# Kernel tuning notes

Hardware: AMD Instinct MI355X
Metric: run time of the kernel (lower is better)

Reference implementation:

```python
import jax, jax.numpy as jnp
import numpy as np

B, D_IN = 16384, 1024
N_DOM, EMB = 4, 16
H1, H2, H3 = 512, 256, 128
FH = 64
EPS = 1e-5


def setup_inputs() -> dict:
    key = jax.random.key(0)
    ks = jax.random.split(key, 32)
    s = 0.02
    def rn(k, shape):
        return jax.random.normal(k, shape, dtype=jnp.float32) * s
    inp = {
        "x": jax.random.normal(ks[0], (B, D_IN), dtype=jnp.float32),
        "domain_ids": jax.random.randint(ks[1], (B,), 0, N_DOM),
        # PartitionedNormalization params
        "pn_w": jnp.ones((N_DOM, D_IN), jnp.float32),
        "pn_b": jnp.zeros((N_DOM, D_IN), jnp.float32),
        # center net: D_IN->512->256->128
        "cW1": rn(ks[2], (D_IN, H1)), "cb1": jnp.zeros((H1,), jnp.float32),
        "cW2": rn(ks[3], (H1, H2)),  "cb2": jnp.zeros((H2,), jnp.float32),
        "cW3": rn(ks[4], (H2, H3)),  "cb3": jnp.zeros((H3,), jnp.float32),
        # domain-specific nets, stacked over domains
        "dW1": rn(ks[5], (N_DOM, D_IN, H1)), "db1": jnp.zeros((N_DOM, H1), jnp.float32),
        "dW2": rn(ks[6], (N_DOM, H1, H2)),  "db2": jnp.zeros((N_DOM, H2), jnp.float32),
        "dW3": rn(ks[7], (N_DOM, H2, H3)),  "db3": jnp.full((N_DOM, H3), 1.0, jnp.float32),  # domain_net_init_bias=1.0
        # final mlp: 128->64->1
        "fW1": rn(ks[8], (H3, FH)), "fb1": jnp.zeros((FH,), jnp.float32),
        "fW2": rn(ks[9], (FH, 1)),  "fb2": jnp.zeros((1,), jnp.float32),
        # domain embedding + auxiliary net: 16->32->1
        "dom_emb": rn(ks[10], (N_DOM, EMB)),
        "aW1": rn(ks[11], (EMB, 32)), "ab1": jnp.zeros((32,), jnp.float32),
        "aW2": rn(ks[12], (32, 1)),   "ab2": jnp.zeros((1,), jnp.float32),
    }
    return inp


def _forward(x, domain_ids, pn_w, pn_b,
             cW1, cb1, cW2, cb2, cW3, cb3,
             dW1, db1, dW2, db2, dW3, db3,
             fW1, fb1, fW2, fb2,
             dom_emb, aW1, ab1, aW2, ab2):
    # Partitioned normalization: per-sample layernorm over features,
    # domain-conditional affine (vectorized gather instead of python loop)
    mean = jnp.mean(x, axis=1, keepdims=True)
    var = jnp.mean(jnp.square(x - mean), axis=1, keepdims=True)  # unbiased=False
    norm = (x - mean) / jnp.sqrt(var + EPS)
    norm = norm * pn_w[domain_ids] + pn_b[domain_ids]  # (B, D_IN)

    # center net
    h = jax.nn.relu(norm @ cW1 + cb1)
    h = jax.nn.relu(h @ cW2 + cb2)
    h_center = h @ cW3 + cb3  # (B, H3)

    # domain-specific nets: compute all domains, then gather per-sample
    hd = jax.nn.relu(jnp.einsum('bi,dio->bdo', norm, dW1) + db1[None])   # (B,D,H1)
    hd = jax.nn.relu(jnp.einsum('bdi,dio->bdo', hd, dW2) + db2[None])    # (B,D,H2)
    hd = jnp.einsum('bdi,dio->bdo', hd, dW3) + db3[None]                 # (B,D,H3)
    h_domain = jnp.take_along_axis(hd, domain_ids[:, None, None], axis=1)[:, 0]  # (B,H3)

    h_fused = h_center * jnp.tanh(h_domain)

    main = jax.nn.relu(h_fused @ fW1 + fb1) @ fW2 + fb2  # (B,1)

    de = dom_emb[domain_ids]                              # (B,EMB)
    aux = jax.nn.relu(de @ aW1 + ab1) @ aW2 + ab2         # (B,1)

    return jax.nn.sigmoid(main + aux)


def reference(x, domain_ids, pn_w, pn_b,
              cW1, cb1, cW2, cb2, cW3, cb3,
              dW1, db1, dW2, db2, dW3, db3,
              fW1, fb1, fW2, fb2,
              dom_emb, aW1, ab1, aW2, ab2):
    return _forward(x, domain_ids, pn_w, pn_b,
                    cW1, cb1, cW2, cb2, cW3, cb3,
                    dW1, db1, dW2, db2, dW3, db3,
                    fW1, fb1, fW2, fb2,
                    dom_emb, aW1, ab1, aW2, ab2)
```

## Files before the change

kernel.cpp:

```cpp
#include <hip/hip_runtime.h>
#include <hip/hip_bf16.h>
#include <stdint.h>

#define NB   16384
#define DIN  1024
#define MPAD 16896

typedef __bf16 bf16;
typedef __bf16 v8bf __attribute__((ext_vector_type(8)));
typedef float  v4f  __attribute__((ext_vector_type(4)));
typedef long   v2l  __attribute__((ext_vector_type(2)));
typedef unsigned char u8;

typedef __attribute__((address_space(1))) void* as1_ptr;
typedef __attribute__((address_space(3))) void* as3_ptr;

__device__ __forceinline__ void gl_lds16(const void* g, void* l) {
  __builtin_amdgcn_global_load_lds((as1_ptr)(g), (as3_ptr)(l), 16, 0, 0);
}

__device__ __forceinline__ unsigned short bfbits(float f) {
  bf16 h = (bf16)f;
  return __builtin_bit_cast(unsigned short, h);
}

__device__ __forceinline__ unsigned short pk8(float a, float b) {
  int u = __builtin_amdgcn_cvt_pk_fp8_f32(a, b, 0, false);
  return (unsigned short)(u & 0xffff);
}

__global__ __launch_bounds__(1024) void k_histscan_aux(
    const int* __restrict__ dom, int* __restrict__ pstart, int* __restrict__ cnt2,
    int* __restrict__ perm, float* __restrict__ aux,
    const float* __restrict__ dom_emb, const float* __restrict__ aW1,
    const float* __restrict__ ab1, const float* __restrict__ aW2,
    const float* __restrict__ ab2) {
  __shared__ int hist[4];
  int tid = threadIdx.x, lane = tid & 63;
  if (tid < 4) hist[tid] = 0;
  if (tid >= 8 && tid < 12) cnt2[tid - 8] = 0;
  for (int j = tid; j < MPAD; j += 1024) perm[j] = -1;
  __syncthreads();
  int c0 = 0, c1 = 0, c2 = 0, c3 = 0;
#pragma unroll
  for (int it = 0; it < 16; it++) {
    int d = dom[it * 1024 + tid];
    c0 += (d == 0); c1 += (d == 1); c2 += (d == 2); c3 += (d == 3);
  }
#pragma unroll
  for (int o = 32; o; o >>= 1) {
    c0 += __shfl_xor(c0, o, 64); c1 += __shfl_xor(c1, o, 64);
    c2 += __shfl_xor(c2, o, 64); c3 += __shfl_xor(c3, o, 64);
  }
  if (lane == 0) {
    atomicAdd(&hist[0], c0); atomicAdd(&hist[1], c1);
    atomicAdd(&hist[2], c2); atomicAdd(&hist[3], c3);
  }
  __syncthreads();
  if (tid == 0) {
    int p = 0;
    for (int d = 0; d < 4; d++) { pstart[d] = p; p += (hist[d] + 127) & ~127; }
    pstart[4] = p;
  }
  if (tid < 4) {
    float a = ab2[0];
    for (int j = 0; j < 32; j++) {
      float s = ab1[j];
      for (int i = 0; i < 16; i++) s += dom_emb[tid * 16 + i] * aW1[i * 32 + j];
      a += fmaxf(s, 0.f) * aW2[j];
    }
    aux[tid] = a;
  }
}

__global__ void k_assign(const int* __restrict__ dom, const int* __restrict__ pstart,
                         int* __restrict__ cnt2, int* __restrict__ perm,
                         int* __restrict__ rowpos) {
  int i = blockIdx.x * 256 + threadIdx.x;
  int lane = threadIdx.x & 63;
  int d = dom[i];
  unsigned long long ltmask = (1ull << lane) - 1ull;
#pragma unroll
  for (int dd = 0; dd < 4; dd++) {
    unsigned long long m = __ballot(d == dd);
    int c = __popcll(m);
    int base = 0;
    if (lane == 0 && c) base = atomicAdd(&cnt2[dd], c);
    base = __shfl(base, 0, 64);
    if (d == dd) {
      int pos = pstart[dd] + base + __popcll(m & ltmask);
      perm[pos] = i;
      rowpos[i] = pos;
    }
  }
}

__global__ __launch_bounds__(256) void k_ln(const float* __restrict__ x,
                                            const int* __restrict__ dom,
                                            const int* __restrict__ rowpos,
                                            const float* __restrict__ pn_w,
                                            const float* __restrict__ pn_b,
                                            u8* __restrict__ norm) {
  int wv = threadIdx.x >> 6, lane = threadIdx.x & 63;
  int r = blockIdx.x * 4 + wv;
  const float* xr = x + (size_t)r * DIN;
  float4 v[4];
#pragma unroll
  for (int g = 0; g < 4; g++) v[g] = *(const float4*)(xr + g * 256 + lane * 4);
  float s = 0.f;
#pragma unroll
  for (int g = 0; g < 4; g++) s += v[g].x + v[g].y + v[g].z + v[g].w;
#pragma unroll
  for (int o = 32; o; o >>= 1) s += __shfl_xor(s, o, 64);
  float mean = s * (1.f / 1024.f);
  float q = 0.f;
#pragma unroll
  for (int g = 0; g < 4; g++) {
    float a = v[g].x - mean, b = v[g].y - mean, c = v[g].z - mean, e = v[g].w - mean;
    q += a * a + b * b + c * c + e * e;
  }
#pragma unroll
  for (int o = 32; o; o >>= 1) q += __shfl_xor(q, o, 64);
  float rstd = rsqrtf(q * (1.f / 1024.f) + 1e-5f);
  int d = dom[r];
  int pos = rowpos[r];
  const float* pw = pn_w + (size_t)d * DIN;
  const float* pb = pn_b + (size_t)d * DIN;
  u8* orow = norm + (size_t)pos * DIN;
#pragma unroll
  for (int g = 0; g < 4; g++) {
    float4 w4 = *(const float4*)(pw + g * 256 + lane * 4);
    float4 b4 = *(const float4*)(pb + g * 256 + lane * 4);
    float f0 = (v[g].x - mean) * rstd * w4.x + b4.x;
    float f1 = (v[g].y - mean) * rstd * w4.y + b4.y;
    float f2 = (v[g].z - mean) * rstd * w4.z + b4.z;
    float f3 = (v[g].w - mean) * rstd * w4.w + b4.w;
    int u = __builtin_amdgcn_cvt_pk_fp8_f32(f0, f1, 0, false);
    u = __builtin_amdgcn_cvt_pk_fp8_f32(f2, f3, u, true);
    *(unsigned int*)(orow + g * 256 + lane * 4) = (unsigned int)u;
  }
}

__global__ __launch_bounds__(256) void k_wt_all(
    const float* __restrict__ cW1, const float* __restrict__ cW2,
    const float* __restrict__ cW3, const float* __restrict__ dW1,
    const float* __restrict__ dW2, const float* __restrict__ dW3,
    const float* __restrict__ fW1,
    u8* __restrict__ cW1t, u8* __restrict__ cW2t, u8* __restrict__ cW3t,
    u8* __restrict__ dW1t, u8* __restrict__ dW2t, u8* __restrict__ dW3t,
    bf16* __restrict__ fW1t) {
  __shared__ float t[64 * 65];
  int bid = blockIdx.x;
  const float* src; u8* dst; int K, N, tile; bool isf = false;
  if (bid < 640) {
    K = 1024; N = 512; int m = bid >> 7; tile = bid & 127;
    src = m == 0 ? cW1 : dW1 + (size_t)(m - 1) * 524288;
    dst = m == 0 ? cW1t : dW1t + (size_t)(m - 1) * 524288;
  } else if (bid < 800) {
    K = 512; N = 256; int m = (bid - 640) >> 5; tile = (bid - 640) & 31;
    src = m == 0 ? cW2 : dW2 + (size_t)(m - 1) * 131072;
    dst = m == 0 ? cW2t : dW2t + (size_t)(m - 1) * 131072;
  } else if (bid < 840) {
    K = 256; N = 128; int m = (bid - 800) >> 3; tile = (bid - 800) & 7;
    src = m == 0 ? cW3 : dW3 + (size_t)(m - 1) * 32768;
    dst = m == 0 ? cW3t : dW3t + (size_t)(m - 1) * 32768;
  } else {
    K = 128; N = 64; tile = bid - 840; src = fW1; dst = nullptr; isf = true;
  }
  int ntn = N >> 6;
  int k0 = (tile / ntn) << 6, n0 = (tile % ntn) << 6;
  int tid = threadIdx.x;
  int r = tid >> 2, c4 = (tid & 3) << 4;
#pragma unroll
  for (int j4 = 0; j4 < 4; j4++) {
    float4 v = *(const float4*)(src + (size_t)(k0 + r) * N + n0 + c4 + j4 * 4);
    t[r * 65 + c4 + j4 * 4 + 0] = v.x;
    t[r * 65 + c4 + j4 * 4 + 1] = v.y;
    t[r * 65 + c4 + j4 * 4 + 2] = v.z;
    t[r * 65 + c4 + j4 * 4 + 3] = v.w;
  }
  __syncthreads();
  int n = tid >> 2, kc = (tid & 3) << 4;
  if (!isf) {
#pragma unroll
    for (int j4 = 0; j4 < 4; j4++) {
      float v0 = t[(kc + j4 * 4 + 0) * 65 + n] * 16.f;
      float v1 = t[(kc + j4 * 4 + 1) * 65 + n] * 16.f;
      float v2 = t[(kc + j4 * 4 + 2) * 65 + n] * 16.f;
      float v3 = t[(kc + j4 * 4 + 3) * 65 + n] * 16.f;
      int u = __builtin_amdgcn_cvt_pk_fp8_f32(v0, v1, 0, false);
      u = __builtin_amdgcn_cvt_pk_fp8_f32(v2, v3, u, true);
      *(unsigned int*)(dst + (size_t)(n0 + n) * K + k0 + kc + j4 * 4) = (unsigned int)u;
    }
  } else {
#pragma unroll
    for (int j4 = 0; j4 < 4; j4++) {
      ushort4 o;
      o.x = bfbits(t[(kc + j4 * 4 + 0) * 65 + n]);
      o.y = bfbits(t[(kc + j4 * 4 + 1) * 65 + n]);
      o.z = bfbits(t[(kc + j4 * 4 + 2) * 65 + n]);
      o.w = bfbits(t[(kc + j4 * 4 + 3) * 65 + n]);
      *(ushort4*)(fW1t + (size_t)(n0 + n) * K + k0 + kc + j4 * 4) = o;
    }
  }
}

__global__ __launch_bounds__(256) void k_gemm(const u8* __restrict__ A, int lda,
                                              int aoffc, int aoffd,
                                              const u8* __restrict__ cWt,
                                              const u8* __restrict__ dWt,
                                              const float* __restrict__ cb,
                                              const float* __restrict__ db,
                                              u8* __restrict__ C, int Nh, int Kd,
                                              int relu, const int* __restrict__ pstart,
                                              int lognct) {
  __shared__ __align__(16) u8 Al[64 * 128];
  __shared__ __align__(16) u8 Bl[128 * 128];
  const int tid = threadIdx.x;
  const int wv = tid >> 6, lane = tid & 63;
  const int nct = 1 << lognct;
  int l = blockIdx.x;
  int t = l >> 3;
  int ct = t & (nct - 1);
  int rt = ((t >> lognct) << 3) | (l & 7);
  const int row0 = rt * 64;
  const int d = (row0 >= pstart[1]) + (row0 >= pstart[2]) + (row0 >= pstart[3]);
  const int n0 = ct * 128;
  const bool isd = (n0 >= Nh);
  const u8* Wt = isd ? dWt + ((size_t)d * Nh + (n0 - Nh)) * Kd : cWt + (size_t)n0 * Kd;
  const float* bias = isd ? db + d * Nh + (n0 - Nh) : cb + n0;
  const int aoff = isd ? aoffd : aoffc;
  const u8* Ab = A + (size_t)row0 * lda + aoff;

  v4f acc[2][4];
#pragma unroll
  for (int i = 0; i < 2; i++)
#pragma unroll
    for (int j = 0; j < 4; j++) acc[i][j] = v4f{0.f, 0.f, 0.f, 0.f};

  const int wm = (wv >> 1) * 32, wn = (wv & 1) * 64;
  const int mrow = lane & 15, quad = lane >> 4;
  const int lrow = lane >> 3;
  const int lchk = lane & 7;
  const int ldc = 2 * Nh;

  for (int kt = 0; kt < Kd; kt += 128) {
#pragma unroll
    for (int p = 0; p < 2; p++) {
      int rbase = wv * 16 + p * 8;
      int r = rbase + lrow;
      int jg = lchk ^ (r & 7);
      gl_lds16(Ab + (size_t)r * lda + kt + jg * 16, &Al[rbase * 128]);
    }
#pragma unroll
    for (int p = 0; p < 4; p++) {
      int rbase = wv * 32 + p * 8;
      int r = rbase + lrow;
      int jg = lchk ^ (r & 7);
      gl_lds16(Wt + (size_t)r * Kd + kt + jg * 16, &Bl[rbase * 128]);
    }
    __syncthreads();
#pragma unroll
    for (int sp = 0; sp < 2; sp++) {
      v2l af[2], bfr[4];
#pragma unroll
      for (int mi = 0; mi < 2; mi++) {
        int m = wm + mi * 16 + mrow;
        int c = (sp * 4 + quad) ^ (m & 7);
        af[mi] = *(const v2l*)&Al[m * 128 + c * 16];
      }
#pragma unroll
      for (int ni = 0; ni < 4; ni++) {
        int n = wn + ni * 16 + mrow;
        int c = (sp * 4 + quad) ^ (n & 7);
        bfr[ni] = *(const v2l*)&Bl[n * 128 + c * 16];
      }
#pragma unroll
      for (int mi = 0; mi < 2; mi++)
#pragma unroll
        for (int ni = 0; ni < 4; ni++)
          acc[mi][ni] =
              __builtin_amdgcn_mfma_f32_16x16x32_fp8_fp8(af[mi].x, bfr[ni].x, acc[mi][ni], 0, 0, 0);
#pragma unroll
      for (int mi = 0; mi < 2; mi++)
#pragma unroll
        for (int ni = 0; ni < 4; ni++)
          acc[mi][ni] =
              __builtin_amdgcn_mfma_f32_16x16x32_fp8_fp8(af[mi].y, bfr[ni].y, acc[mi][ni], 0, 0, 0);
    }
    __syncthreads();
  }

  float bv[4];
#pragma unroll
  for (int ni = 0; ni < 4; ni++) bv[ni] = bias[wn + ni * 16 + mrow];
#pragma unroll
  for (int mi = 0; mi < 2; mi++) {
    int growb = row0 + wm + mi * 16 + quad * 4;
#pragma unroll
    for (int ni = 0; ni < 4; ni++) {
      int gcol = n0 + wn + ni * 16 + mrow;
#pragma unroll
      for (int r2 = 0; r2 < 4; r2++) {
        float v = acc[mi][ni][r2] * 0.0625f + bv[ni];
        if (relu) v = fmaxf(v, 0.f);
        float g = __shfl_xor(v, 1, 64);
        if (!(mrow & 1))
          *(unsigned short*)(C + (size_t)(growb + r2) * ldc + gcol) = pk8(v, g);
      }
    }
  }
}

__global__ __launch_bounds__(256) void k_gemm3(const u8* __restrict__ A,
                                               const u8* __restrict__ cW3t,
                                               const u8* __restrict__ dW3t,
                                               const float* __restrict__ cb3,
                                               const float* __restrict__ db3,
                                               const bf16* __restrict__ fW1t,
                                               const float* __restrict__ fb1,
                                               const float* __restrict__ fW2,
                                               const float* __restrict__ fb2,
                                               const int* __restrict__ perm,
                                               const int* __restrict__ pstart,
                                               const float* __restrict__ aux,
                                               float* __restrict__ out) {
  __shared__ __align__(16) u8 Al[64 * 128];
  __shared__ __align__(16) u8 Bl[128 * 128];
  __shared__ __align__(16) bf16 fusedL[64 * 128];
  __shared__ __align__(16) bf16 fwB[64 * 128];
  const int tid = threadIdx.x, wv = tid >> 6, lane = tid & 63;
  const int row0 = blockIdx.x * 64;
  const int d = (row0 >= pstart[1]) + (row0 >= pstart[2]) + (row0 >= pstart[3]);
  const u8* Ab = A + (size_t)row0 * 512;
  const int mrow = lane & 15, quad = lane >> 4;
  const int lrow = lane >> 3, lchk = lane & 7;
  const int wm = (wv >> 1) * 32, wn = (wv & 1) * 64;

  {
    int c = lane & 15, rsub = lane >> 4;
#pragma unroll
    for (int p = 0; p < 4; p++) {
      int rbase = wv * 16 + p * 4;
      int row = rbase + rsub;
      int g = (c & 8) | ((c ^ row) & 7);
      gl_lds16(fW1t + row * 128 + g * 8, &fwB[rbase * 128]);
    }
  }

  v4f accC[2][4], accD[2][4];
#pragma unroll
  for (int i = 0; i < 2; i++)
#pragma unroll
    for (int j = 0; j < 4; j++) { accC[i][j] = v4f{0.f,0.f,0.f,0.f}; accD[i][j] = v4f{0.f,0.f,0.f,0.f}; }

#pragma unroll
  for (int ph = 0; ph < 2; ph++) {
    const u8* Wt = ph ? dW3t + (size_t)d * 32768 : cW3t;
    const int aoff = ph * 256;
    for (int kt = 0; kt < 256; kt += 128) {
#pragma unroll
      for (int p = 0; p < 2; p++) {
        int rbase = wv * 16 + p * 8;
        int r = rbase + lrow;
        int jg = lchk ^ (r & 7);
        gl_lds16(Ab + (size_t)r * 512 + aoff + kt + jg * 16, &Al[rbase * 128]);
      }
#pragma unroll
      for (int p = 0; p < 4; p++) {
        int rbase = wv * 32 + p * 8;
        int r = rbase + lrow;
        int jg = lchk ^ (r & 7);
        gl_lds16(Wt + (size_t)r * 256 + kt + jg * 16, &Bl[rbase * 128]);
      }
      __syncthreads();
#pragma unroll
      for (int sp = 0; sp < 2; sp++) {
        v2l af[2], bfr[4];
#pragma unroll
        for (int mi = 0; mi < 2; mi++) {
          int m = wm + mi * 16 + mrow;
          int c = (sp * 4 + quad) ^ (m & 7);
          af[mi] = *(const v2l*)&Al[m * 128 + c * 16];
        }
#pragma unroll
        for (int ni = 0; ni < 4; ni++) {
          int n = wn + ni * 16 + mrow;
          int c = (sp * 4 + quad) ^ (n & 7);
          bfr[ni] = *(const v2l*)&Bl[n * 128 + c * 16];
        }
        if (ph == 0) {
#pragma unroll
          for (int mi = 0; mi < 2; mi++)
#pragma unroll
            for (int ni = 0; ni < 4; ni++) {
              accC[mi][ni] = __builtin_amdgcn_mfma_f32_16x16x32_fp8_fp8(af[mi].x, bfr[ni].x, accC[mi][ni], 0, 0, 0);
              accC[mi][ni] = __builtin_amdgcn_mfma_f32_16x16x32_fp8_fp8(af[mi].y, bfr[ni].y, accC[mi][ni], 0, 0, 0);
            }
        } else {
#pragma unroll
          for (int mi = 0; mi < 2; mi++)
#pragma unroll
            for (int ni = 0; ni < 4; ni++) {
              accD[mi][ni] = __builtin_amdgcn_mfma_f32_16x16x32_fp8_fp8(af[mi].x, bfr[ni].x, accD[mi][ni], 0, 0, 0);
              accD[mi][ni] = __builtin_amdgcn_mfma_f32_16x16x32_fp8_fp8(af[mi].y, bfr[ni].y, accD[mi][ni], 0, 0, 0);
            }
        }
      }
      __syncthreads();
    }
  }

#pragma unroll
  for (int mi = 0; mi < 2; mi++) {
    int rowb = wm + mi * 16 + quad * 4;
#pragma unroll
    for (int ni = 0; ni < 4; ni++) {
      int col = wn + ni * 16 + mrow;
      float cbv = cb3[col];
      float dbv = db3[d * 128 + col];
      int jc = col >> 3, coff = col & 7;
#pragma unroll
      for (int r2 = 0; r2 < 4; r2++) {
        int rr = rowb + r2;
        float f = (accC[mi][ni][r2] * 0.0625f + cbv) * tanhf(accD[mi][ni][r2] * 0.0625f + dbv);
        int cs = (jc & 8) | ((jc ^ rr) & 7);
        fusedL[rr * 128 + cs * 8 + coff] = (bf16)f;
      }
    }
  }
  __syncthreads();

  float fb1v[4], fW2v[4];
#pragma unroll
  for (int nt = 0; nt < 4; nt++) {
    int col = nt * 16 + mrow;
    fb1v[nt] = fb1[col];
    fW2v[nt] = fW2[col];
  }
  v4f hacc[4];
#pragma unroll
  for (int nt = 0; nt < 4; nt++) hacc[nt] = v4f{0.f, 0.f, 0.f, 0.f};
  const int m = wv * 16 + mrow;
#pragma unroll
  for (int s = 0; s < 4; s++) {
    int j = s * 4 + quad;
    int ca = (j & 8) | ((j ^ m) & 7);
    v8bf af = *(const v8bf*)&fusedL[m * 128 + ca * 8];
#pragma unroll
    for (int nt = 0; nt < 4; nt++) {
      int n = nt * 16 + mrow;
      int cbk = (j & 8) | ((j ^ n) & 7);
      v8bf bfr = *(const v8bf*)&fwB[n * 128 + cbk * 8];
      hacc[nt] = __builtin_amdgcn_mfma_f32_16x16x32_bf16(af, bfr, hacc[nt], 0, 0, 0);
    }
  }
  float ys[4];
#pragma unroll
  for (int r2 = 0; r2 < 4; r2++) {
    float s = 0.f;
#pragma unroll
    for (int nt = 0; nt < 4; nt++) s += fmaxf(hacc[nt][r2] + fb1v[nt], 0.f) * fW2v[nt];
    ys[r2] = s;
  }
#pragma unroll
  for (int o = 1; o < 16; o <<= 1)
#pragma unroll
    for (int r2 = 0; r2 < 4; r2++) ys[r2] += __shfl_xor(ys[r2], o, 64);
  if (mrow == 0) {
    const float addc = fb2[0] + aux[d];
#pragma unroll
    for (int r2 = 0; r2 < 4; r2++) {
      int prow = row0 + wv * 16 + quad * 4 + r2;
      int orig = perm[prow];
      if (orig >= 0) out[orig] = 1.f / (1.f + expf(-(ys[r2] + addc)));
    }
  }
}

extern "C" void kernel_launch(void* const* d_in, const int* in_sizes, int n_in,
                              void* d_out, int out_size, void* d_ws, size_t ws_size,
                              hipStream_t stream) {
  (void)in_sizes; (void)n_in; (void)out_size; (void)ws_size;
  const float* x      = (const float*)d_in[0];
  const int*   dom    = (const int*)d_in[1];
  const float* pn_w   = (const float*)d_in[2];
  const float* pn_b   = (const float*)d_in[3];
  const float* cW1    = (const float*)d_in[4];
  const float* cb1    = (const float*)d_in[5];
  const float* cW2    = (const float*)d_in[6];
  const float* cb2    = (const float*)d_in[7];
  const float* cW3    = (const float*)d_in[8];
  const float* cb3    = (const float*)d_in[9];
  const float* dW1    = (const float*)d_in[10];
  const float* db1    = (const float*)d_in[11];
  const float* dW2    = (const float*)d_in[12];
  const float* db2    = (const float*)d_in[13];
  const float* dW3    = (const float*)d_in[14];
  const float* db3    = (const float*)d_in[15];
  const float* fW1    = (const float*)d_in[16];
  const float* fb1    = (const float*)d_in[17];
  const float* fW2    = (const float*)d_in[18];
  const float* fb2    = (const float*)d_in[19];
  const float* demb   = (const float*)d_in[20];
  const float* aW1    = (const float*)d_in[21];
  const float* ab1    = (const float*)d_in[22];
  const float* aW2    = (const float*)d_in[23];
  const float* ab2    = (const float*)d_in[24];
  float* out = (float*)d_out;

  char* w = (char*)d_ws;
  int*   cnt2   = (int*)(w + 0);
  int*   pstart = (int*)(w + 32);
  float* aux    = (float*)(w + 64);
  int*   perm   = (int*)(w + 256);
  int*   rowpos = (int*)(w + 67840);
  u8*    bufA   = (u8*)(w + 133376);
  u8*    bufB   = (u8*)(w + 17434880);
  u8*    cW1t   = (u8*)(w + 34736384);
  u8*    cW2t   = (u8*)(w + 35260672);
  u8*    cW3t   = (u8*)(w + 35391744);
  u8*    dW1t   = (u8*)(w + 35424512);
  u8*    dW2t   = (u8*)(w + 37521664);
  u8*    dW3t   = (u8*)(w + 38045952);
  bf16*  fW1t   = (bf16*)(w + 38177024);

  k_histscan_aux<<<1, 1024, 0, stream>>>(dom, pstart, cnt2, perm, aux,
                                         demb, aW1, ab1, aW2, ab2);
  k_assign<<<64, 256, 0, stream>>>(dom, pstart, cnt2, perm, rowpos);
  k_ln<<<4096, 256, 0, stream>>>(x, dom, rowpos, pn_w, pn_b, bufA);
  k_wt_all<<<842, 256, 0, stream>>>(cW1, cW2, cW3, dW1, dW2, dW3, fW1,
                                    cW1t, cW2t, cW3t, dW1t, dW2t, dW3t, fW1t);

  k_gemm<<<2112, 256, 0, stream>>>(bufA, 1024, 0, 0, cW1t, dW1t, cb1, db1,
                                   bufB, 512, 1024, 1, pstart, 3);
  k_gemm<<<1056, 256, 0, stream>>>(bufB, 1024, 0, 512, cW2t, dW2t, cb2, db2,
                                   bufA, 256, 512, 1, pstart, 2);
  k_gemm3<<<264, 256, 0, stream>>>(bufA, cW3t, dW3t, cb3, db3, fW1t,
                                   fb1, fW2, fb2, perm, pstart, aux, out);
}
```

Measured before the change: 235.1 us.

## Use K=128 scaled FP8 MFMA and parallelize histogram prologue

The GEMM inner loops switch from pairs of 16x16x32 FP8 MFMAs to a single 16x16x128 scaled FP8 MFMA (f8f6f4 with unit scales) per tile, loading 32 contiguous bytes per lane from the swizzled LDS. This cuts MFMA issue count and LDS-read instruction count per K-tile. The single-block histogram/scan/aux kernel is split into a 64-block ballot histogram plus a tiny scan kernel. Counter zeroing and the aux MLP move into a spare block of the weight-transpose kernel, which now runs first. The new path relies on the operand layout of the larger MFMA matching the per-lane chunk selection, and it adds one extra kernel launch.

```diff
diff --git a/kernel.cpp b/kernel.cpp
--- a/kernel.cpp
+++ b/kernel.cpp
@@ -9,7 +9,8 @@
 typedef __bf16 bf16;
 typedef __bf16 v8bf __attribute__((ext_vector_type(8)));
 typedef float  v4f  __attribute__((ext_vector_type(4)));
-typedef long   v2l  __attribute__((ext_vector_type(2)));
+typedef int    v4i  __attribute__((ext_vector_type(4)));
+typedef int    v8i  __attribute__((ext_vector_type(8)));
 typedef unsigned char u8;
 
 typedef __attribute__((address_space(1))) void* as1_ptr;
@@ -29,47 +30,31 @@
   return (unsigned short)(u & 0xffff);
 }
 
-__global__ __launch_bounds__(1024) void k_histscan_aux(
-    const int* __restrict__ dom, int* __restrict__ pstart, int* __restrict__ cnt2,
-    int* __restrict__ perm, float* __restrict__ aux,
-    const float* __restrict__ dom_emb, const float* __restrict__ aW1,
-    const float* __restrict__ ab1, const float* __restrict__ aW2,
-    const float* __restrict__ ab2) {
-  __shared__ int hist[4];
-  int tid = threadIdx.x, lane = tid & 63;
-  if (tid < 4) hist[tid] = 0;
-  if (tid >= 8 && tid < 12) cnt2[tid - 8] = 0;
-  for (int j = tid; j < MPAD; j += 1024) perm[j] = -1;
-  __syncthreads();
-  int c0 = 0, c1 = 0, c2 = 0, c3 = 0;
-#pragma unroll
-  for (int it = 0; it < 16; it++) {
-    int d = dom[it * 1024 + tid];
-    c0 += (d == 0); c1 += (d == 1); c2 += (d == 2); c3 += (d == 3);
-  }
-#pragma unroll
-  for (int o = 32; o; o >>= 1) {
-    c0 += __shfl_xor(c0, o, 64); c1 += __shfl_xor(c1, o, 64);
-    c2 += __shfl_xor(c2, o, 64); c3 += __shfl_xor(c3, o, 64);
-  }
-  if (lane == 0) {
-    atomicAdd(&hist[0], c0); atomicAdd(&hist[1], c1);
-    atomicAdd(&hist[2], c2); atomicAdd(&hist[3], c3);
-  }
-  __syncthreads();
-  if (tid == 0) {
+__device__ __forceinline__ v4f mfma_fp8_k128(v8i a, v8i b, v4f c) {
+  return __builtin_amdgcn_mfma_scale_f32_16x16x128_f8f6f4(a, b, c, 0, 0,
+                                                          0, 127u, 0, 127u);
+}
+
+__global__ __launch_bounds__(256) void k_hist(const int* __restrict__ dom,
+                                              int* __restrict__ hist,
+                                              int* __restrict__ perm) {
+  int tid = threadIdx.x, b = blockIdx.x;
+  int i = b * 256 + tid, lane = tid & 63;
+  int d = dom[i];
+#pragma unroll
+  for (int dd = 0; dd < 4; dd++) {
+    unsigned long long m = __ballot(d == dd);
+    if (lane == 0 && m) atomicAdd(&hist[dd], __popcll(m));
+  }
+  for (int j = b * 264 + tid; j < b * 264 + 264; j += 256)
+    if (j < MPAD) perm[j] = -1;
+}
+
+__global__ void k_scan(const int* __restrict__ hist, int* __restrict__ pstart) {
+  if (threadIdx.x == 0) {
     int p = 0;
     for (int d = 0; d < 4; d++) { pstart[d] = p; p += (hist[d] + 127) & ~127; }
     pstart[4] = p;
-  }
-  if (tid < 4) {
-    float a = ab2[0];
-    for (int j = 0; j < 32; j++) {
-      float s = ab1[j];
-      for (int i = 0; i < 16; i++) s += dom_emb[tid * 16 + i] * aW1[i * 32 + j];
-      a += fmaxf(s, 0.f) * aW2[j];
-    }
-    aux[tid] = a;
   }
 }
 
@@ -148,9 +133,27 @@
     const float* __restrict__ fW1,
     u8* __restrict__ cW1t, u8* __restrict__ cW2t, u8* __restrict__ cW3t,
     u8* __restrict__ dW1t, u8* __restrict__ dW2t, u8* __restrict__ dW3t,
-    bf16* __restrict__ fW1t) {
+    bf16* __restrict__ fW1t,
+    const float* __restrict__ dom_emb, const float* __restrict__ aW1,
+    const float* __restrict__ ab1, const float* __restrict__ aW2,
+    const float* __restrict__ ab2, int* __restrict__ histz,
+    float* __restrict__ aux) {
   __shared__ float t[64 * 65];
   int bid = blockIdx.x;
+  int tid = threadIdx.x;
+  if (bid == 841) {
+    if (tid < 8) histz[tid] = 0;
+    if (tid >= 64 && tid < 68) {
+      int dd = tid - 64;
+      float a = ab2[0];
+      for (int j = 0; j < 32; j++) {
+        float s = ab1[j];
+        for (int i = 0; i < 16; i++) s += dom_emb[dd * 16 + i] * aW1[i * 32 + j];
+        a += fmaxf(s, 0.f) * aW2[j];
+      }
+      aux[dd] = a;
+    }
+  }
   const float* src; u8* dst; int K, N, tile; bool isf = false;
   if (bid < 640) {
     K = 1024; N = 512; int m = bid >> 7; tile = bid & 127;
@@ -169,7 +172,6 @@
   }
   int ntn = N >> 6;
   int k0 = (tile / ntn) << 6, n0 = (tile % ntn) << 6;
-  int tid = threadIdx.x;
   int r = tid >> 2, c4 = (tid & 3) << 4;
 #pragma unroll
   for (int j4 = 0; j4 < 4; j4++) {
@@ -260,34 +262,30 @@
       gl_lds16(Wt + (size_t)r * Kd + kt + jg * 16, &Bl[rbase * 128]);
     }
     __syncthreads();
-#pragma unroll
-    for (int sp = 0; sp < 2; sp++) {
-      v2l af[2], bfr[4];
-#pragma unroll
-      for (int mi = 0; mi < 2; mi++) {
-        int m = wm + mi * 16 + mrow;
-        int c = (sp * 4 + quad) ^ (m & 7);
-        af[mi] = *(const v2l*)&Al[m * 128 + c * 16];
-      }
-#pragma unroll
-      for (int ni = 0; ni < 4; ni++) {
-        int n = wn + ni * 16 + mrow;
-        int c = (sp * 4 + quad) ^ (n & 7);
-        bfr[ni] = *(const v2l*)&Bl[n * 128 + c * 16];
-      }
-#pragma unroll
-      for (int mi = 0; mi < 2; mi++)
-#pragma unroll
-        for (int ni = 0; ni < 4; ni++)
-          acc[mi][ni] =
-              __builtin_amdgcn_mfma_f32_16x16x32_fp8_fp8(af[mi].x, bfr[ni].x, acc[mi][ni], 0, 0, 0);
-#pragma unroll
-      for (int mi = 0; mi < 2; mi++)
-#pragma unroll
-        for (int ni = 0; ni < 4; ni++)
-          acc[mi][ni] =
-              __builtin_amdgcn_mfma_f32_16x16x32_fp8_fp8(af[mi].y, bfr[ni].y, acc[mi][ni], 0, 0, 0);
-    }
+    v8i af[2], bfr[4];
+#pragma unroll
+    for (int mi = 0; mi < 2; mi++) {
+      int m = wm + mi * 16 + mrow;
+      int s0 = (2 * quad) ^ (m & 7);
+      int s1 = (2 * quad + 1) ^ (m & 7);
+      v4i lo = *(const v4i*)&Al[m * 128 + s0 * 16];
+      v4i hi = *(const v4i*)&Al[m * 128 + s1 * 16];
+      af[mi] = __builtin_shufflevector(lo, hi, 0, 1, 2, 3, 4, 5, 6, 7);
+    }
+#pragma unroll
+    for (int ni = 0; ni < 4; ni++) {
+      int n = wn + ni * 16 + mrow;
+      int s0 = (2 * quad) ^ (n & 7);
+      int s1 = (2 * quad + 1) ^ (n & 7);
+      v4i lo = *(const v4i*)&Bl[n * 128 + s0 * 16];
+      v4i hi = *(const v4i*)&Bl[n * 128 + s1 * 16];
+      bfr[ni] = __builtin_shufflevector(lo, hi, 0, 1, 2, 3, 4, 5, 6, 7);
+    }
+#pragma unroll
+    for (int mi = 0; mi < 2; mi++)
+#pragma unroll
+      for (int ni = 0; ni < 4; ni++)
+        acc[mi][ni] = mfma_fp8_k128(af[mi], bfr[ni], acc[mi][ni]);
     __syncthreads();
   }
 
@@ -374,38 +372,37 @@
         gl_lds16(Wt + (size_t)r * 256 + kt + jg * 16, &Bl[rbase * 128]);
       }
       __syncthreads();
-#pragma unroll
-      for (int sp = 0; sp < 2; sp++) {
-        v2l af[2], bfr[4];
-#pragma unroll
-        for (int mi = 0; mi < 2; mi++) {
-          int m = wm + mi * 16 + mrow;
-          int c = (sp * 4 + quad) ^ (m & 7);
-          af[mi] = *(const v2l*)&Al[m * 128 + c * 16];
-        }
-#pragma unroll
-        for (int ni = 0; ni < 4; ni++) {
-          int n = wn + ni * 16 + mrow;
-          int c = (sp * 4 + quad) ^ (n & 7);
-          bfr[ni] = *(const v2l*)&Bl[n * 128 + c * 16];
-        }
-        if (ph == 0) {
-#pragma unroll
-          for (int mi = 0; mi < 2; mi++)
-#pragma unroll
-            for (int ni = 0; ni < 4; ni++) {
-              accC[mi][ni] = __builtin_amdgcn_mfma_f32_16x16x32_fp8_fp8(af[mi].x, bfr[ni].x, accC[mi][ni], 0, 0, 0);
-              accC[mi][ni] = __builtin_amdgcn_mfma_f32_16x16x32_fp8_fp8(af[mi].y, bfr[ni].y, accC[mi][ni], 0, 0, 0);
-            }
-        } else {
-#pragma unroll
-          for (int mi = 0; mi < 2; mi++)
-#pragma unroll
-            for (int ni = 0; ni < 4; ni++) {
-              accD[mi][ni] = __builtin_amdgcn_mfma_f32_16x16x32_fp8_fp8(af[mi].x, bfr[ni].x, accD[mi][ni], 0, 0, 0);
-              accD[mi][ni] = __builtin_amdgcn_mfma_f32_16x16x32_fp8_fp8(af[mi].y, bfr[ni].y, accD[mi][ni], 0, 0, 0);
-            }
-        }
+      v8i af[2], bfr[4];
+#pragma unroll
+      for (int mi = 0; mi < 2; mi++) {
+        int m = wm + mi * 16 + mrow;
+        int s0 = (2 * quad) ^ (m & 7);
+        int s1 = (2 * quad + 1) ^ (m & 7);
+        v4i lo = *(const v4i*)&Al[m * 128 + s0 * 16];
+        v4i hi = *(const v4i*)&Al[m * 128 + s1 * 16];
+        af[mi] = __builtin_shufflevector(lo, hi, 0, 1, 2, 3, 4, 5, 6, 7);
+      }
+#pragma unroll
+      for (int ni = 0; ni < 4; ni++) {
+        int n = wn + ni * 16 + mrow;
+        int s0 = (2 * quad) ^ (n & 7);
+        int s1 = (2 * quad + 1) ^ (n & 7);
+        v4i lo = *(const v4i*)&Bl[n * 128 + s0 * 16];
+        v4i hi = *(const v4i*)&Bl[n * 128 + s1 * 16];
+        bfr[ni] = __builtin_shufflevector(lo, hi, 0, 1, 2, 3, 4, 5, 6, 7);
+      }
+      if (ph == 0) {
+#pragma unroll
+        for (int mi = 0; mi < 2; mi++)
+#pragma unroll
+          for (int ni = 0; ni < 4; ni++)
+            accC[mi][ni] = mfma_fp8_k128(af[mi], bfr[ni], accC[mi][ni]);
+      } else {
+#pragma unroll
+        for (int mi = 0; mi < 2; mi++)
+#pragma unroll
+          for (int ni = 0; ni < 4; ni++)
+            accD[mi][ni] = mfma_fp8_k128(af[mi], bfr[ni], accD[mi][ni]);
       }
       __syncthreads();
     }
@@ -510,7 +507,8 @@
   float* out = (float*)d_out;
 
   char* w = (char*)d_ws;
-  int*   cnt2   = (int*)(w + 0);
+  int*   histz  = (int*)(w + 0);
+  int*   cnt2   = (int*)(w + 16);
   int*   pstart = (int*)(w + 32);
   float* aux    = (float*)(w + 64);
   int*   perm   = (int*)(w + 256);
@@ -525,12 +523,13 @@
   u8*    dW3t   = (u8*)(w + 38045952);
   bf16*  fW1t   = (bf16*)(w + 38177024);
 
-  k_histscan_aux<<<1, 1024, 0, stream>>>(dom, pstart, cnt2, perm, aux,
-                                         demb, aW1, ab1, aW2, ab2);
+  k_wt_all<<<842, 256, 0, stream>>>(cW1, cW2, cW3, dW1, dW2, dW3, fW1,
+                                    cW1t, cW2t, cW3t, dW1t, dW2t, dW3t, fW1t,
+                                    demb, aW1, ab1, aW2, ab2, histz, aux);
+  k_hist<<<64, 256, 0, stream>>>(dom, histz, perm);
+  k_scan<<<1, 64, 0, stream>>>(histz, pstart);
   k_assign<<<64, 256, 0, stream>>>(dom, pstart, cnt2, perm, rowpos);
   k_ln<<<4096, 256, 0, stream>>>(x, dom, rowpos, pn_w, pn_b, bufA);
-  k_wt_all<<<842, 256, 0, stream>>>(cW1, cW2, cW3, dW1, dW2, dW3, fW1,
-                                    cW1t, cW2t, cW3t, dW1t, dW2t, dW3t, fW1t);
 
   k_gemm<<<2112, 256, 0, stream>>>(bufA, 1024, 0, 0, cW1t, dW1t, cb1, db1,
                                    bufB, 512, 1024, 1, pstart, 3);
```

New measurement: 241.8 us. 1.03x slower.

## Split center and domain layer-3 GEMMs across two warp groups in k_gemm3

Applied to the files above, without the earlier changes.

k_gemm3 now runs 512 threads. Waves 0-3 compute the center-net third layer and waves 4-7 compute the domain-net third layer at the same time, each with its own LDS tiles, where before both ran one after the other in a single group of four waves. The center output and the tanh of the domain output are written to separate LDS buffers, and the first four waves multiply them before the fused final MLP. The change doubles the parallelism of a small-grid kernel (264 blocks) and shortens its serial chain. In exchange it uses more LDS per block, leaves half the waves idle during the final MLP, and adds an extra bf16 rounding step before the product.

```diff
diff --git a/kernel.cpp b/kernel.cpp
--- a/kernel.cpp
+++ b/kernel.cpp
@@ -312,7 +312,7 @@
   }
 }
 
-__global__ __launch_bounds__(256) void k_gemm3(const u8* __restrict__ A,
+__global__ __launch_bounds__(512) void k_gemm3(const u8* __restrict__ A,
                                                const u8* __restrict__ cW3t,
                                                const u8* __restrict__ dW3t,
                                                const float* __restrict__ cb3,
@@ -325,155 +325,155 @@
                                                const int* __restrict__ pstart,
                                                const float* __restrict__ aux,
                                                float* __restrict__ out) {
-  __shared__ __align__(16) u8 Al[64 * 128];
-  __shared__ __align__(16) u8 Bl[128 * 128];
-  __shared__ __align__(16) bf16 fusedL[64 * 128];
-  __shared__ __align__(16) bf16 fwB[64 * 128];
+  __shared__ __align__(16) u8 smem[49152];
   const int tid = threadIdx.x, wv = tid >> 6, lane = tid & 63;
+  const int ph = wv >> 2, wvp = wv & 3;
   const int row0 = blockIdx.x * 64;
   const int d = (row0 >= pstart[1]) + (row0 >= pstart[2]) + (row0 >= pstart[3]);
-  const u8* Ab = A + (size_t)row0 * 512;
+  const u8* Ab = A + (size_t)row0 * 512 + ph * 256;
+  const u8* Wt = ph ? dW3t + (size_t)d * 32768 : cW3t;
+  u8* myAl = smem + ph * 8192;
+  u8* myBl = smem + 16384 + ph * 16384;
   const int mrow = lane & 15, quad = lane >> 4;
   const int lrow = lane >> 3, lchk = lane & 7;
-  const int wm = (wv >> 1) * 32, wn = (wv & 1) * 64;
+  const int wm = (wvp >> 1) * 32, wn = (wvp & 1) * 64;
+
+  v4f acc[2][4];
+#pragma unroll
+  for (int i = 0; i < 2; i++)
+#pragma unroll
+    for (int j = 0; j < 4; j++) acc[i][j] = v4f{0.f, 0.f, 0.f, 0.f};
+
+  for (int kt = 0; kt < 256; kt += 128) {
+#pragma unroll
+    for (int p = 0; p < 2; p++) {
+      int rbase = wvp * 16 + p * 8;
+      int r = rbase + lrow;
+      int jg = lchk ^ (r & 7);
+      gl_lds16(Ab + (size_t)r * 512 + kt + jg * 16, &myAl[rbase * 128]);
+    }
+#pragma unroll
+    for (int p = 0; p < 4; p++) {
+      int rbase = wvp * 32 + p * 8;
+      int r = rbase + lrow;
+      int jg = lchk ^ (r & 7);
+      gl_lds16(Wt + (size_t)r * 256 + kt + jg * 16, &myBl[rbase * 128]);
+    }
+    __syncthreads();
+#pragma unroll
+    for (int sp = 0; sp < 2; sp++) {
+      v2l af[2], bfr[4];
+#pragma unroll
+      for (int mi = 0; mi < 2; mi++) {
+        int m = wm + mi * 16 + mrow;
+        int c = (sp * 4 + quad) ^ (m & 7);
+        af[mi] = *(const v2l*)&myAl[m * 128 + c * 16];
+      }
+#pragma unroll
+      for (int ni = 0; ni < 4; ni++) {
+        int n = wn + ni * 16 + mrow;
+        int c = (sp * 4 + quad) ^ (n & 7);
+        bfr[ni] = *(const v2l*)&myBl[n * 128 + c * 16];
+      }
+#pragma unroll
+      for (int mi = 0; mi < 2; mi++)
+#pragma unroll
+        for (int ni = 0; ni < 4; ni++) {
+          acc[mi][ni] = __builtin_amdgcn_mfma_f32_16x16x32_fp8_fp8(af[mi].x, bfr[ni].x, acc[mi][ni], 0, 0, 0);
+          acc[mi][ni] = __builtin_amdgcn_mfma_f32_16x16x32_fp8_fp8(af[mi].y, bfr[ni].y, acc[mi][ni], 0, 0, 0);
+        }
+    }
+    __syncthreads();
+  }
+
+  bf16* fwB    = (bf16*)(smem);
+  bf16* fusedC = (bf16*)(smem + 16384);
+  bf16* fusedT = (bf16*)(smem + 32768);
 
   {
     int c = lane & 15, rsub = lane >> 4;
 #pragma unroll
-    for (int p = 0; p < 4; p++) {
-      int rbase = wv * 16 + p * 4;
+    for (int p = 0; p < 2; p++) {
+      int rbase = wv * 8 + p * 4;
       int row = rbase + rsub;
       int g = (c & 8) | ((c ^ row) & 7);
       gl_lds16(fW1t + row * 128 + g * 8, &fwB[rbase * 128]);
     }
   }
 
-  v4f accC[2][4], accD[2][4];
-#pragma unroll
-  for (int i = 0; i < 2; i++)
-#pragma unroll
-    for (int j = 0; j < 4; j++) { accC[i][j] = v4f{0.f,0.f,0.f,0.f}; accD[i][j] = v4f{0.f,0.f,0.f,0.f}; }
-
-#pragma unroll
-  for (int ph = 0; ph < 2; ph++) {
-    const u8* Wt = ph ? dW3t + (size_t)d * 32768 : cW3t;
-    const int aoff = ph * 256;
-    for (int kt = 0; kt < 256; kt += 128) {
-#pragma unroll
-      for (int p = 0; p < 2; p++) {
-        int rbase = wv * 16 + p * 8;
-        int r = rbase + lrow;
-        int jg = lchk ^ (r & 7);
-        gl_lds16(Ab + (size_t)r * 512 + aoff + kt + jg * 16, &Al[rbase * 128]);
-      }
-#pragma unroll
-      for (int p = 0; p < 4; p++) {
-        int rbase = wv * 32 + p * 8;
-        int r = rbase + lrow;
-        int jg = lchk ^ (r & 7);
-        gl_lds16(Wt + (size_t)r * 256 + kt + jg * 16, &Bl[rbase * 128]);
-      }
-      __syncthreads();
-#pragma unroll
-      for (int sp = 0; sp < 2; sp++) {
-        v2l af[2], bfr[4];
-#pragma unroll
-        for (int mi = 0; mi < 2; mi++) {
-          int m = wm + mi * 16 + mrow;
-          int c = (sp * 4 + quad) ^ (m & 7);
-          af[mi] = *(const v2l*)&Al[m * 128 + c * 16];
+  {
+    bf16* dstF = ph ? fusedT : fusedC;
+    const float* bias = ph ? db3 + d * 128 : cb3;
+#pragma unroll
+    for (int mi = 0; mi < 2; mi++) {
+      int rowb = wm + mi * 16 + quad * 4;
+#pragma unroll
+      for (int ni = 0; ni < 4; ni++) {
+        int col = wn + ni * 16 + mrow;
+        float bv = bias[col];
+        int jc = col >> 3, coff = col & 7;
+#pragma unroll
+        for (int r2 = 0; r2 < 4; r2++) {
+          int rr = rowb + r2;
+          float h = acc[mi][ni][r2] * 0.0625f + bv;
+          float f = ph ? tanhf(h) : h;
+          int cs = (jc & 8) | ((jc ^ rr) & 7);
+          dstF[rr * 128 + cs * 8 + coff] = (bf16)f;
         }
-#pragma unroll
-        for (int ni = 0; ni < 4; ni++) {
-          int n = wn + ni * 16 + mrow;
-          int c = (sp * 4 + quad) ^ (n & 7);
-          bfr[ni] = *(const v2l*)&Bl[n * 128 + c * 16];
-        }
-        if (ph == 0) {
-#pragma unroll
-          for (int mi = 0; mi < 2; mi++)
-#pragma unroll
-            for (int ni = 0; ni < 4; ni++) {
-              accC[mi][ni] = __builtin_amdgcn_mfma_f32_16x16x32_fp8_fp8(af[mi].x, bfr[ni].x, accC[mi][ni], 0, 0, 0);
-              accC[mi][ni] = __builtin_amdgcn_mfma_f32_16x16x32_fp8_fp8(af[mi].y, bfr[ni].y, accC[mi][ni], 0, 0, 0);
-            }
-        } else {
-#pragma unroll
-          for (int mi = 0; mi < 2; mi++)
-#pragma unroll
-            for (int ni = 0; ni < 4; ni++) {
-              accD[mi][ni] = __builtin_amdgcn_mfma_f32_16x16x32_fp8_fp8(af[mi].x, bfr[ni].x, accD[mi][ni], 0, 0, 0);
-              accD[mi][ni] = __builtin_amdgcn_mfma_f32_16x16x32_fp8_fp8(af[mi].y, bfr[ni].y, accD[mi][ni], 0, 0, 0);
-            }
-        }
-      }
-      __syncthreads();
-    }
-  }
-
-#pragma unroll
-  for (int mi = 0; mi < 2; mi++) {
-    int rowb = wm + mi * 16 + quad * 4;
-#pragma unroll
-    for (int ni = 0; ni < 4; ni++) {
-      int col = wn + ni * 16 + mrow;
-      float cbv = cb3[col];
-      float dbv = db3[d * 128 + col];
-      int jc = col >> 3, coff = col & 7;
+      }
+    }
+  }
+  __syncthreads();
+
+  if (wv < 4) {
+    float fb1v[4], fW2v[4];
+#pragma unroll
+    for (int nt = 0; nt < 4; nt++) {
+      int col = nt * 16 + mrow;
+      fb1v[nt] = fb1[col];
+      fW2v[nt] = fW2[col];
+    }
+    v4f hacc[4];
+#pragma unroll
+    for (int nt = 0; nt < 4; nt++) hacc[nt] = v4f{0.f, 0.f, 0.f, 0.f};
+    const int m = wv * 16 + mrow;
+#pragma unroll
+    for (int s = 0; s < 4; s++) {
+      int j = s * 4 + quad;
+      int ca = (j & 8) | ((j ^ m) & 7);
+      v8bf a1 = *(const v8bf*)&fusedC[m * 128 + ca * 8];
+      v8bf a2 = *(const v8bf*)&fusedT[m * 128 + ca * 8];
+      v8bf af;
+#pragma unroll
+      for (int e = 0; e < 8; e++) af[e] = (bf16)((float)a1[e] * (float)a2[e]);
+#pragma unroll
+      for (int nt = 0; nt < 4; nt++) {
+        int n = nt * 16 + mrow;
+        int cbk = (j & 8) | ((j ^ n) & 7);
+        v8bf bfr = *(const v8bf*)&fwB[n * 128 + cbk * 8];
+        hacc[nt] = __builtin_amdgcn_mfma_f32_16x16x32_bf16(af, bfr, hacc[nt], 0, 0, 0);
+      }
+    }
+    float ys[4];
+#pragma unroll
+    for (int r2 = 0; r2 < 4; r2++) {
+      float s = 0.f;
+#pragma unroll
+      for (int nt = 0; nt < 4; nt++) s += fmaxf(hacc[nt][r2] + fb1v[nt], 0.f) * fW2v[nt];
+      ys[r2] = s;
+    }
+#pragma unroll
+    for (int o = 1; o < 16; o <<= 1)
+#pragma unroll
+      for (int r2 = 0; r2 < 4; r2++) ys[r2] += __shfl_xor(ys[r2], o, 64);
+    if (mrow == 0) {
+      const float addc = fb2[0] + aux[d];
 #pragma unroll
       for (int r2 = 0; r2 < 4; r2++) {
-        int rr = rowb + r2;
-        float f = (accC[mi][ni][r2] * 0.0625f + cbv) * tanhf(accD[mi][ni][r2] * 0.0625f + dbv);
-        int cs = (jc & 8) | ((jc ^ rr) & 7);
-        fusedL[rr * 128 + cs * 8 + coff] = (bf16)f;
-      }
-    }
-  }
-  __syncthreads();
-
-  float fb1v[4], fW2v[4];
-#pragma unroll
-  for (int nt = 0; nt < 4; nt++) {
-    int col = nt * 16 + mrow;
-    fb1v[nt] = fb1[col];
-    fW2v[nt] = fW2[col];
-  }
-  v4f hacc[4];
-#pragma unroll
-  for (int nt = 0; nt < 4; nt++) hacc[nt] = v4f{0.f, 0.f, 0.f, 0.f};
-  const int m = wv * 16 + mrow;
-#pragma unroll
-  for (int s = 0; s < 4; s++) {
-    int j = s * 4 + quad;
-    int ca = (j & 8) | ((j ^ m) & 7);
-    v8bf af = *(const v8bf*)&fusedL[m * 128 + ca * 8];
-#pragma unroll
-    for (int nt = 0; nt < 4; nt++) {
-      int n = nt * 16 + mrow;
-      int cbk = (j & 8) | ((j ^ n) & 7);
-      v8bf bfr = *(const v8bf*)&fwB[n * 128 + cbk * 8];
-      hacc[nt] = __builtin_amdgcn_mfma_f32_16x16x32_bf16(af, bfr, hacc[nt], 0, 0, 0);
-    }
-  }
-  float ys[4];
-#pragma unroll
-  for (int r2 = 0; r2 < 4; r2++) {
-    float s = 0.f;
-#pragma unroll
-    for (int nt = 0; nt < 4; nt++) s += fmaxf(hacc[nt][r2] + fb1v[nt], 0.f) * fW2v[nt];
-    ys[r2] = s;
-  }
-#pragma unroll
-  for (int o = 1; o < 16; o <<= 1)
-#pragma unroll
-    for (int r2 = 0; r2 < 4; r2++) ys[r2] += __shfl_xor(ys[r2], o, 64);
-  if (mrow == 0) {
-    const float addc = fb2[0] + aux[d];
-#pragma unroll
-    for (int r2 = 0; r2 < 4; r2++) {
-      int prow = row0 + wv * 16 + quad * 4 + r2;
-      int orig = perm[prow];
-      if (orig >= 0) out[orig] = 1.f / (1.f + expf(-(ys[r2] + addc)));
+        int prow = row0 + wv * 16 + quad * 4 + r2;
+        int orig = perm[prow];
+        if (orig >= 0) out[orig] = 1.f / (1.f + expf(-(ys[r2] + addc)));
+      }
     }
   }
 }
@@ -510,7 +510,7 @@
   float* out = (float*)d_out;
 
   char* w = (char*)d_ws;
-  int*   cnt2   = (int*)(w + 0);
+  int*   cnt2   = (int*)(w + 16);
   int*   pstart = (int*)(w + 32);
   float* aux    = (float*)(w + 64);
   int*   perm   = (int*)(w + 256);
@@ -536,6 +536,6 @@
                                    bufB, 512, 1024, 1, pstart, 3);
   k_gemm<<<1056, 256, 0, stream>>>(bufB, 1024, 0, 512, cW2t, dW2t, cb2, db2,
                                    bufA, 256, 512, 1, pstart, 2);
-  k_gemm3<<<264, 256, 0, stream>>>(bufA, cW3t, dW3t, cb3, db3, fW1t,
+  k_gemm3<<<264, 512, 0, stream>>>(bufA, cW3t, dW3t, cb3, db3, fW1t,
                                    fb1, fW2, fb2, perm, pstart, aux, out);
 }
```

Measured after the change: 238.4 us. Within noise of the previous version (+1.4%).
